# Optimization experiments

Hardware: AMD Instinct MI355X
Metric: run time of the kernel (lower is better)

The kernel has to match this reference:

```python
import jax, jax.numpy as jnp
import numpy as np

N, E, H, ED, GD = 100000, 1600000, 128, 64, 64
LN_EPS = 1e-5


def setup_inputs() -> dict:
    key = jax.random.key(0)
    ks = jax.random.split(key, 16)
    s = lambda d: 1.0 / np.sqrt(d)
    return {
        "node_state": jax.random.normal(ks[0], (N, H), jnp.float32),
        "edge_index": jax.random.randint(ks[1], (2, E), 0, N, jnp.int64),
        "edge_state": jax.random.normal(ks[2], (E, ED), jnp.float32),
        "global_state": jax.random.normal(ks[3], (GD,), jnp.float32),
        "msg_w1": jax.random.normal(ks[4], (H + ED + GD, H), jnp.float32) * s(H + ED + GD),
        "msg_b1": jnp.zeros((H,), jnp.float32),
        "msg_w2": jax.random.normal(ks[5], (H, H), jnp.float32) * s(H),
        "msg_b2": jnp.zeros((H,), jnp.float32),
        "upd_w1": jax.random.normal(ks[6], (2 * H + GD, H), jnp.float32) * s(2 * H + GD),
        "upd_b1": jnp.zeros((H,), jnp.float32),
        "upd_w2": jax.random.normal(ks[7], (H, H), jnp.float32) * s(H),
        "upd_b2": jnp.zeros((H,), jnp.float32),
        "ln_gamma": jnp.ones((H,), jnp.float32),
        "ln_beta": jnp.zeros((H,), jnp.float32),
    }


def _mlp(x, w1, b1, w2, b2):
    return jax.nn.relu(x @ w1 + b1) @ w2 + b2


def reference(node_state, edge_index, edge_state, global_state,
              msg_w1, msg_b1, msg_w2, msg_b2,
              upd_w1, upd_b1, upd_w2, upd_b2,
              ln_gamma, ln_beta):
    src, dst = edge_index[0], edge_index[1]
    num_nodes = node_state.shape[0]
    num_edges = src.shape[0]

    global_edges = jnp.broadcast_to(global_state, (num_edges, global_state.shape[0]))
    message_input = jnp.concatenate([node_state[src], edge_state, global_edges], axis=-1)
    messages = _mlp(message_input, msg_w1, msg_b1, msg_w2, msg_b2)  # [E, H]

    aggregated = jax.ops.segment_sum(messages, dst, num_segments=num_nodes)  # [N, H]
    degree = jax.ops.segment_sum(jnp.ones((num_edges,), node_state.dtype), dst,
                                 num_segments=num_nodes)  # [N]
    aggregated = aggregated / jnp.maximum(degree, 1.0)[:, None]

    global_nodes = jnp.broadcast_to(global_state, (num_nodes, global_state.shape[0]))
    update_input = jnp.concatenate([node_state, aggregated, global_nodes], axis=-1)
    delta = _mlp(update_input, upd_w1, upd_b1, upd_w2, upd_b2)

    x = node_state + delta
    mu = jnp.mean(x, axis=-1, keepdims=True)
    var = jnp.mean(jnp.square(x - mu), axis=-1, keepdims=True)
    return (x - mu) * jax.lax.rsqrt(var + LN_EPS) * ln_gamma + ln_beta
```

## Files before the change

### kernel.cpp

```cpp
#include <hip/hip_runtime.h>
#include <hip/hip_bf16.h>
#include <stdint.h>

#define NN 100000
#define NE 1600000

typedef __attribute__((ext_vector_type(4))) float f32x4;
typedef __attribute__((ext_vector_type(8))) __bf16 bf16x8;
typedef __attribute__((ext_vector_type(8))) short s16x8;
typedef __attribute__((ext_vector_type(4))) unsigned int u32x4;

__device__ __forceinline__ unsigned short f2bf(float f) {
  unsigned int u = __builtin_bit_cast(unsigned int, f);
  u += 0x7fffu + ((u >> 16) & 1u);
  return (unsigned short)(u >> 16);
}

__device__ __forceinline__ f32x4 mfma16(bf16x8 a, bf16x8 b, f32x4 c) {
  return __builtin_amdgcn_mfma_f32_16x16x32_bf16(a, b, c, 0, 0, 0);
}

__global__ void convert_kernel(const float* __restrict__ w1, const float* __restrict__ w2,
                               const float* __restrict__ g,
                               unsigned short* __restrict__ w1b, unsigned short* __restrict__ w2b,
                               unsigned short* __restrict__ gb)
{
  const int tid = blockIdx.x * 256 + threadIdx.x;
  if (tid < 256 * 128) w1b[tid] = f2bf(w1[tid]);
  if (tid < 128 * 128) w2b[tid] = f2bf(w2[tid]);
  if (tid < 64) gb[tid] = f2bf(g[tid]);
}

__global__ __launch_bounds__(256, 2) void edge_kernel(
    const int* __restrict__ ei,
    const float* __restrict__ edge_state,
    const float* __restrict__ node_state,
    const unsigned short* __restrict__ w1b,
    const unsigned short* __restrict__ w2b,
    const float* __restrict__ bias1g,
    const float* __restrict__ bias2g,
    const unsigned short* __restrict__ gb,
    float* __restrict__ agg,
    float* __restrict__ deg)
{
  __shared__ unsigned short sX[64 * 256];
  __shared__ unsigned short sH[64 * 128];
  __shared__ int sDst[64];

  const int t = threadIdx.x;
  const int lane = t & 63;
  const int wv = t >> 6;
  const int l15 = lane & 15;
  const int lq = lane >> 4;

  bf16x8 b1f[8][2], b2f[4][2];
  float bs1[2], bs2[2];
  for (int n = 0; n < 2; ++n) {
    const int col = wv * 32 + n * 16 + l15;
    bs1[n] = bias1g[col];
    bs2[n] = bias2g[col];
    for (int ks = 0; ks < 8; ++ks) {
      const int k0 = ks * 32 + lq * 8;
      s16x8 v;
#pragma unroll
      for (int j = 0; j < 8; ++j) v[j] = (short)w1b[(k0 + j) * 128 + col];
      b1f[ks][n] = __builtin_bit_cast(bf16x8, v);
    }
    for (int ks = 0; ks < 4; ++ks) {
      const int k0 = ks * 32 + lq * 8;
      s16x8 v;
#pragma unroll
      for (int j = 0; j < 8; ++j) v[j] = (short)w2b[(k0 + j) * 128 + col];
      b2f[ks][n] = __builtin_bit_cast(bf16x8, v);
    }
  }

  const int r = t >> 2;
  const int p = t & 3;
  const int rs = r & 7;

  for (int tile = blockIdx.x; tile < NE / 64; tile += gridDim.x) {
    __syncthreads();
    const int e0 = tile * 64;

    const int src = ei[e0 + r];
    if (p == 0) {
      const int d = ei[NE + e0 + r];
      sDst[r] = d;
      atomicAdd(&deg[d], 1.0f);
    }
    {
      const f32x4* nsv = (const f32x4*)(node_state + (size_t)src * 128 + p * 32);
#pragma unroll
      for (int j = 0; j < 4; ++j) {
        f32x4 x0 = nsv[2 * j], x1 = nsv[2 * j + 1];
        unsigned short buf[8];
#pragma unroll
        for (int i = 0; i < 4; ++i) { buf[i] = f2bf(x0[i]); buf[4 + i] = f2bf(x1[i]); }
        const int c = p * 4 + j;
        *(u32x4*)((char*)sX + r * 512 + ((c ^ rs) * 16)) = *(u32x4*)buf;
      }
    }
    {
      const f32x4* es = (const f32x4*)(edge_state + (size_t)e0 * 64 + r * 64 + p * 16);
      f32x4 e0v = es[0], e1v = es[1], e2v = es[2], e3v = es[3];
      unsigned short bufa[8], bufb[8];
#pragma unroll
      for (int i = 0; i < 4; ++i) {
        bufa[i] = f2bf(e0v[i]); bufa[4 + i] = f2bf(e1v[i]);
        bufb[i] = f2bf(e2v[i]); bufb[4 + i] = f2bf(e3v[i]);
      }
      const int c = 16 + 2 * p;
      *(u32x4*)((char*)sX + r * 512 + ((c ^ rs) * 16)) = *(u32x4*)bufa;
      *(u32x4*)((char*)sX + r * 512 + (((c + 1) ^ rs) * 16)) = *(u32x4*)bufb;
    }
    {
      const u32x4* g = (const u32x4*)(gb + p * 16);
      const int c = 24 + 2 * p;
      *(u32x4*)((char*)sX + r * 512 + ((c ^ rs) * 16)) = g[0];
      *(u32x4*)((char*)sX + r * 512 + (((c + 1) ^ rs) * 16)) = g[1];
    }
    __syncthreads();

    f32x4 acc[4][2];
#pragma unroll
    for (int m = 0; m < 4; ++m)
#pragma unroll
      for (int n = 0; n < 2; ++n)
        acc[m][n] = (f32x4){bs1[n], bs1[n], bs1[n], bs1[n]};
#pragma unroll
    for (int ks = 0; ks < 8; ++ks) {
      bf16x8 a[4];
#pragma unroll
      for (int m = 0; m < 4; ++m) {
        const int row = m * 16 + l15;
        a[m] = *(const bf16x8*)((const char*)sX + row * 512 + (((4 * ks + lq) ^ (row & 7)) * 16));
      }
#pragma unroll
      for (int m = 0; m < 4; ++m)
#pragma unroll
        for (int n = 0; n < 2; ++n)
          acc[m][n] = mfma16(a[m], b1f[ks][n], acc[m][n]);
    }
#pragma unroll
    for (int m = 0; m < 4; ++m)
#pragma unroll
      for (int n = 0; n < 2; ++n)
#pragma unroll
        for (int i = 0; i < 4; ++i) {
          const int row = m * 16 + lq * 4 + i;
          const int col = wv * 32 + n * 16 + l15;
          float v = acc[m][n][i];
          v = v > 0.f ? v : 0.f;
          *(unsigned short*)((char*)sH + row * 256 +
                             ((((col >> 3) ^ (row & 7)) * 16) + (col & 7) * 2)) = f2bf(v);
        }
    __syncthreads();

    f32x4 acc2[4][2];
#pragma unroll
    for (int m = 0; m < 4; ++m)
#pragma unroll
      for (int n = 0; n < 2; ++n)
        acc2[m][n] = (f32x4){bs2[n], bs2[n], bs2[n], bs2[n]};
#pragma unroll
    for (int ks = 0; ks < 4; ++ks) {
      bf16x8 a[4];
#pragma unroll
      for (int m = 0; m < 4; ++m) {
        const int row = m * 16 + l15;
        a[m] = *(const bf16x8*)((const char*)sH + row * 256 + (((4 * ks + lq) ^ (row & 7)) * 16));
      }
#pragma unroll
      for (int m = 0; m < 4; ++m)
#pragma unroll
        for (int n = 0; n < 2; ++n)
          acc2[m][n] = mfma16(a[m], b2f[ks][n], acc2[m][n]);
    }
#pragma unroll
    for (int m = 0; m < 4; ++m)
#pragma unroll
      for (int i = 0; i < 4; ++i) {
        const int row = m * 16 + lq * 4 + i;
        const int d = sDst[row];
#pragma unroll
        for (int n = 0; n < 2; ++n) {
          const int col = wv * 32 + n * 16 + l15;
          atomicAdd(&agg[(size_t)d * 128 + col], acc2[m][n][i]);
        }
      }
  }
}

__global__ __launch_bounds__(128, 3) void upd1_kernel(
    const float* __restrict__ node_state,
    const float* __restrict__ agg,
    const float* __restrict__ deg,
    const float* __restrict__ u1,
    const float* __restrict__ b1,
    const float* __restrict__ gs,
    float* __restrict__ h1out)
{
  const int n = blockIdx.x * 128 + threadIdx.x;
  const bool act = n < NN;
  const size_t row = (size_t)(act ? n : 0) * 128;

  f32x4 acc[32];
#pragma unroll
  for (int c = 0; c < 32; ++c) acc[c] = *(const f32x4*)(b1 + 4 * c);

  const float rdeg = act ? (1.0f / fmaxf(deg[n], 1.0f)) : 0.0f;

  for (int k4 = 0; k4 < 32; ++k4) {
    const f32x4 x = *(const f32x4*)(node_state + row + 4 * k4);
#pragma unroll
    for (int kk = 0; kk < 4; ++kk) {
      const float xk = x[kk];
      const float* wr = u1 + (size_t)(4 * k4 + kk) * 128;
#pragma unroll
      for (int c = 0; c < 32; ++c) acc[c] += xk * *(const f32x4*)(wr + 4 * c);
    }
  }
  for (int k4 = 0; k4 < 32; ++k4) {
    const f32x4 x = *(const f32x4*)(agg + row + 4 * k4);
#pragma unroll
    for (int kk = 0; kk < 4; ++kk) {
      const float xk = x[kk] * rdeg;
      const float* wr = u1 + (size_t)(128 + 4 * k4 + kk) * 128;
#pragma unroll
      for (int c = 0; c < 32; ++c) acc[c] += xk * *(const f32x4*)(wr + 4 * c);
    }
  }
  for (int k = 0; k < 64; ++k) {
    const float xk = gs[k];
    const float* wr = u1 + (size_t)(256 + k) * 128;
#pragma unroll
    for (int c = 0; c < 32; ++c) acc[c] += xk * *(const f32x4*)(wr + 4 * c);
  }

  if (act) {
    float* o = h1out + (size_t)n * 128;
#pragma unroll
    for (int c = 0; c < 32; ++c) {
      f32x4 v = acc[c];
#pragma unroll
      for (int i = 0; i < 4; ++i) v[i] = v[i] > 0.f ? v[i] : 0.f;
      *(f32x4*)(o + 4 * c) = v;
    }
  }
}

__global__ __launch_bounds__(128, 3) void upd2_kernel(
    const float* __restrict__ node_state,
    const float* __restrict__ h1,
    const float* __restrict__ u2,
    const float* __restrict__ b2,
    const float* __restrict__ lng,
    const float* __restrict__ lnb,
    float* __restrict__ out)
{
  const int n = blockIdx.x * 128 + threadIdx.x;
  const bool act = n < NN;
  const size_t row = (size_t)(act ? n : 0) * 128;

  f32x4 acc[32];
#pragma unroll
  for (int c = 0; c < 32; ++c) acc[c] = *(const f32x4*)(b2 + 4 * c);

  for (int k4 = 0; k4 < 32; ++k4) {
    const f32x4 h = *(const f32x4*)(h1 + row + 4 * k4);
#pragma unroll
    for (int kk = 0; kk < 4; ++kk) {
      const float hk = h[kk];
      const float* wr = u2 + (size_t)(4 * k4 + kk) * 128;
#pragma unroll
      for (int c = 0; c < 32; ++c) acc[c] += hk * *(const f32x4*)(wr + 4 * c);
    }
  }

  if (act) {
    float s = 0.f, s2 = 0.f;
#pragma unroll
    for (int c = 0; c < 32; ++c) {
      const f32x4 nd = *(const f32x4*)(node_state + row + 4 * c);
      f32x4 x = nd + acc[c];
      acc[c] = x;
#pragma unroll
      for (int i = 0; i < 4; ++i) { s += x[i]; s2 += x[i] * x[i]; }
    }
    const float mu = s * (1.0f / 128.0f);
    float var = s2 * (1.0f / 128.0f) - mu * mu;
    var = var < 0.f ? 0.f : var;
    const float rstd = rsqrtf(var + 1e-5f);
    float* o = out + (size_t)n * 128;
#pragma unroll
    for (int c = 0; c < 32; ++c) {
      const f32x4 g = *(const f32x4*)(lng + 4 * c);
      const f32x4 b = *(const f32x4*)(lnb + 4 * c);
      f32x4 x = acc[c];
#pragma unroll
      for (int i = 0; i < 4; ++i) x[i] = (x[i] - mu) * rstd * g[i] + b[i];
      *(f32x4*)(o + 4 * c) = x;
    }
  }
}

extern "C" void kernel_launch(void* const* d_in, const int* in_sizes, int n_in,
                              void* d_out, int out_size, void* d_ws, size_t ws_size,
                              hipStream_t stream)
{
  const float* node_state = (const float*)d_in[0];
  const int* ei           = (const int*)d_in[1];
  const float* edge_state = (const float*)d_in[2];
  const float* gstate     = (const float*)d_in[3];
  const float* msg_w1     = (const float*)d_in[4];
  const float* msg_b1     = (const float*)d_in[5];
  const float* msg_w2     = (const float*)d_in[6];
  const float* msg_b2     = (const float*)d_in[7];
  const float* upd_w1     = (const float*)d_in[8];
  const float* upd_b1     = (const float*)d_in[9];
  const float* upd_w2     = (const float*)d_in[10];
  const float* upd_b2     = (const float*)d_in[11];
  const float* ln_g       = (const float*)d_in[12];
  const float* ln_b       = (const float*)d_in[13];

  char* ws = (char*)d_ws;
  float* agg              = (float*)(ws + 0);
  float* deg              = (float*)(ws + 51200000);
  float* h1buf            = (float*)(ws + 51600000);
  unsigned short* w1b     = (unsigned short*)(ws + 102800000);
  unsigned short* w2b     = (unsigned short*)(ws + 102865536);
  unsigned short* gb      = (unsigned short*)(ws + 102898304);
  (void)ws_size; (void)in_sizes; (void)n_in; (void)out_size;

  hipMemsetAsync(ws, 0, 51600000, stream);
  hipLaunchKernelGGL(convert_kernel, dim3(128), dim3(256), 0, stream,
                     msg_w1, msg_w2, gstate, w1b, w2b, gb);
  hipLaunchKernelGGL(edge_kernel, dim3(512), dim3(256), 0, stream,
                     ei, edge_state, node_state, w1b, w2b, msg_b1, msg_b2, gb, agg, deg);
  hipLaunchKernelGGL(upd1_kernel, dim3((NN + 127) / 128), dim3(128), 0, stream,
                     node_state, agg, deg, upd_w1, upd_b1, gstate, h1buf);
  hipLaunchKernelGGL(upd2_kernel, dim3((NN + 127) / 128), dim3(128), 0, stream,
                     node_state, h1buf, upd_w2, upd_b2, ln_g, ln_b, (float*)d_out);
}
```

Before: 1.167 ms.

## Sort edges by destination via CSR and pre-reduce messages before atomics

Builds a destination-sorted edge permutation (histogram, single-block scan, atomic scatter) and has the edge kernel process edges in that order. Each tile stages its messages in shared memory and run-length sums them per destination column, so there are far fewer float atomics into the aggregate buffer. Degree now comes from the integer histogram. The cost is three extra kernels, one of them a serial single-block scan, plus gathered rather than streaming edge_state reads. Occupancy is raised to 3 blocks per SM with a larger grid.

```diff
diff --git a/kernel.cpp b/kernel.cpp
--- a/kernel.cpp
+++ b/kernel.cpp
@@ -31,21 +31,74 @@
   if (tid < 64) gb[tid] = f2bf(g[tid]);
 }
 
-__global__ __launch_bounds__(256, 2) void edge_kernel(
+__global__ void hist_kernel(const int* __restrict__ ei, int* __restrict__ cnt)
+{
+  int i = blockIdx.x * 256 + threadIdx.x;
+  const int stride = gridDim.x * 256;
+  for (; i < NE; i += stride) atomicAdd(&cnt[ei[NE + i]], 1);
+}
+
+__global__ __launch_bounds__(1024) void scan_kernel(const int* __restrict__ cnt,
+                                                    int* __restrict__ row_start,
+                                                    int* __restrict__ cursor)
+{
+  __shared__ int part[1024];
+  const int t = threadIdx.x;
+  const int chunk = (NN + 1023) / 1024;
+  const int base = t * chunk;
+  int s = 0;
+  for (int i = 0; i < chunk; ++i) {
+    const int idx = base + i;
+    if (idx < NN) s += cnt[idx];
+  }
+  part[t] = s;
+  __syncthreads();
+  for (int off = 1; off < 1024; off <<= 1) {
+    int v = (t >= off) ? part[t - off] : 0;
+    __syncthreads();
+    part[t] += v;
+    __syncthreads();
+  }
+  int run = (t == 0) ? 0 : part[t - 1];
+  for (int i = 0; i < chunk; ++i) {
+    const int idx = base + i;
+    if (idx < NN) {
+      row_start[idx] = run;
+      cursor[idx] = run;
+      run += cnt[idx];
+    }
+  }
+}
+
+__global__ void scatter_kernel(const int* __restrict__ ei, int* __restrict__ cursor,
+                               int* __restrict__ csr)
+{
+  int i = blockIdx.x * 256 + threadIdx.x;
+  const int stride = gridDim.x * 256;
+  for (; i < NE; i += stride) {
+    const int d = ei[NE + i];
+    const int pos = atomicAdd(&cursor[d], 1);
+    csr[pos] = i;
+  }
+}
+
+__global__ __launch_bounds__(256, 3) void edge_kernel(
     const int* __restrict__ ei,
     const float* __restrict__ edge_state,
     const float* __restrict__ node_state,
+    const int* __restrict__ csr,
     const unsigned short* __restrict__ w1b,
     const unsigned short* __restrict__ w2b,
     const float* __restrict__ bias1g,
     const float* __restrict__ bias2g,
     const unsigned short* __restrict__ gb,
-    float* __restrict__ agg,
-    float* __restrict__ deg)
+    float* __restrict__ agg)
 {
   __shared__ unsigned short sX[64 * 256];
   __shared__ unsigned short sH[64 * 128];
   __shared__ int sDst[64];
+  __shared__ int sEid[64];
+  float* sMsgF = (float*)sX;
 
   const int t = threadIdx.x;
   const int lane = t & 63;
@@ -81,14 +134,12 @@
 
   for (int tile = blockIdx.x; tile < NE / 64; tile += gridDim.x) {
     __syncthreads();
-    const int e0 = tile * 64;
-
-    const int src = ei[e0 + r];
-    if (p == 0) {
-      const int d = ei[NE + e0 + r];
-      sDst[r] = d;
-      atomicAdd(&deg[d], 1.0f);
-    }
+    if (t < 64) sEid[t] = csr[tile * 64 + t];
+    __syncthreads();
+
+    const int e = sEid[r];
+    const int src = ei[e];
+    if (p == 0) sDst[r] = ei[NE + e];
     {
       const f32x4* nsv = (const f32x4*)(node_state + (size_t)src * 128 + p * 32);
 #pragma unroll
@@ -102,7 +153,7 @@
       }
     }
     {
-      const f32x4* es = (const f32x4*)(edge_state + (size_t)e0 * 64 + r * 64 + p * 16);
+      const f32x4* es = (const f32x4*)(edge_state + (size_t)e * 64 + p * 16);
       f32x4 e0v = es[0], e1v = es[1], e2v = es[2], e3v = es[3];
       unsigned short bufa[8], bufb[8];
 #pragma unroll
@@ -180,22 +231,39 @@
 #pragma unroll
     for (int m = 0; m < 4; ++m)
 #pragma unroll
-      for (int i = 0; i < 4; ++i) {
-        const int row = m * 16 + lq * 4 + i;
-        const int d = sDst[row];
-#pragma unroll
-        for (int n = 0; n < 2; ++n) {
+      for (int n = 0; n < 2; ++n)
+#pragma unroll
+        for (int i = 0; i < 4; ++i) {
+          const int row = m * 16 + lq * 4 + i;
           const int col = wv * 32 + n * 16 + l15;
-          atomicAdd(&agg[(size_t)d * 128 + col], acc2[m][n][i]);
+          sMsgF[row * 128 + (col ^ row)] = acc2[m][n][i];
         }
+    __syncthreads();
+
+    {
+      const int col = t & 127;
+      const int base = (t >> 7) * 32;
+      float run = 0.f;
+      int prevd = sDst[base];
+      for (int j = 0; j < 32; ++j) {
+        const int rr = base + j;
+        const int d = sDst[rr];
+        if (d != prevd) {
+          atomicAdd(&agg[(size_t)prevd * 128 + col], run);
+          run = 0.f;
+          prevd = d;
+        }
+        run += sMsgF[rr * 128 + (col ^ rr)];
       }
+      atomicAdd(&agg[(size_t)prevd * 128 + col], run);
+    }
   }
 }
 
 __global__ __launch_bounds__(128, 3) void upd1_kernel(
     const float* __restrict__ node_state,
     const float* __restrict__ agg,
-    const float* __restrict__ deg,
+    const int* __restrict__ cnt,
     const float* __restrict__ u1,
     const float* __restrict__ b1,
     const float* __restrict__ gs,
@@ -209,7 +277,7 @@
 #pragma unroll
   for (int c = 0; c < 32; ++c) acc[c] = *(const f32x4*)(b1 + 4 * c);
 
-  const float rdeg = act ? (1.0f / fmaxf(deg[n], 1.0f)) : 0.0f;
+  const float rdeg = act ? (1.0f / (float)max(cnt[n], 1)) : 0.0f;
 
   for (int k4 = 0; k4 < 32; ++k4) {
     const f32x4 x = *(const f32x4*)(node_state + row + 4 * k4);
@@ -326,8 +394,11 @@
 
   char* ws = (char*)d_ws;
   float* agg              = (float*)(ws + 0);
-  float* deg              = (float*)(ws + 51200000);
+  int* cnt                = (int*)(ws + 51200000);
   float* h1buf            = (float*)(ws + 51600000);
+  int* csr                = (int*)(ws + 51600000);
+  int* row_start          = (int*)(ws + 58000000);
+  int* cursor             = (int*)(ws + 58400000);
   unsigned short* w1b     = (unsigned short*)(ws + 102800000);
   unsigned short* w2b     = (unsigned short*)(ws + 102865536);
   unsigned short* gb      = (unsigned short*)(ws + 102898304);
@@ -336,10 +407,13 @@
   hipMemsetAsync(ws, 0, 51600000, stream);
   hipLaunchKernelGGL(convert_kernel, dim3(128), dim3(256), 0, stream,
                      msg_w1, msg_w2, gstate, w1b, w2b, gb);
-  hipLaunchKernelGGL(edge_kernel, dim3(512), dim3(256), 0, stream,
-                     ei, edge_state, node_state, w1b, w2b, msg_b1, msg_b2, gb, agg, deg);
+  hipLaunchKernelGGL(hist_kernel, dim3(2048), dim3(256), 0, stream, ei, cnt);
+  hipLaunchKernelGGL(scan_kernel, dim3(1), dim3(1024), 0, stream, cnt, row_start, cursor);
+  hipLaunchKernelGGL(scatter_kernel, dim3(2048), dim3(256), 0, stream, ei, cursor, csr);
+  hipLaunchKernelGGL(edge_kernel, dim3(768), dim3(256), 0, stream,
+                     ei, edge_state, node_state, csr, w1b, w2b, msg_b1, msg_b2, gb, agg);
   hipLaunchKernelGGL(upd1_kernel, dim3((NN + 127) / 128), dim3(128), 0, stream,
-                     node_state, agg, deg, upd_w1, upd_b1, gstate, h1buf);
+                     node_state, agg, cnt, upd_w1, upd_b1, gstate, h1buf);
   hipLaunchKernelGGL(upd2_kernel, dim3((NN + 127) / 128), dim3(128), 0, stream,
                      node_state, h1buf, upd_w2, upd_b2, ln_g, ln_b, (float*)d_out);
 }
```

Result: slower. 2.390 ms (+104.7%).

## Replace global atomic scatter with bucketed fp8 message staging and LDS aggregation

Applied to the files above, without the earlier changes.

The edge kernel no longer does float atomicAdds into the global aggregate. It converts each message to fp8, appends it to a per-destination bucket of 64 nodes (capacity 1536 per bucket) and records the low destination bits. A new agg kernel then sums each bucket in shared memory and writes the aggregate and integer degree once per node. Node state is also pre-converted to bf16, and the next tile's gathers are prefetched in registers to overlap loads with MFMA work. The trade-offs are fp8 quantisation error in the messages, edges silently dropped if a bucket overflows its fixed capacity, and a large extra workspace buffer for the staged messages.

```diff
diff --git a/kernel.cpp b/kernel.cpp
--- a/kernel.cpp
+++ b/kernel.cpp
@@ -4,8 +4,11 @@
 
 #define NN 100000
 #define NE 1600000
+#define NBK 1563
+#define BCAP 1536
 
 typedef __attribute__((ext_vector_type(4))) float f32x4;
+typedef __attribute__((ext_vector_type(2))) float f32x2;
 typedef __attribute__((ext_vector_type(8))) __bf16 bf16x8;
 typedef __attribute__((ext_vector_type(8))) short s16x8;
 typedef __attribute__((ext_vector_type(4))) unsigned int u32x4;
@@ -20,28 +23,33 @@
   return __builtin_amdgcn_mfma_f32_16x16x32_bf16(a, b, c, 0, 0, 0);
 }
 
-__global__ void convert_kernel(const float* __restrict__ w1, const float* __restrict__ w2,
+__global__ void convert_kernel(const float* __restrict__ ns,
+                               const float* __restrict__ w1, const float* __restrict__ w2,
                                const float* __restrict__ g,
+                               unsigned short* __restrict__ node_bf,
                                unsigned short* __restrict__ w1b, unsigned short* __restrict__ w2b,
                                unsigned short* __restrict__ gb)
 {
   const int tid = blockIdx.x * 256 + threadIdx.x;
+  const int stride = gridDim.x * 256;
+  for (int i = tid; i < NN * 128; i += stride) node_bf[i] = f2bf(ns[i]);
   if (tid < 256 * 128) w1b[tid] = f2bf(w1[tid]);
   if (tid < 128 * 128) w2b[tid] = f2bf(w2[tid]);
   if (tid < 64) gb[tid] = f2bf(g[tid]);
 }
 
-__global__ __launch_bounds__(256, 2) void edge_kernel(
+__global__ __launch_bounds__(256, 3) void edge_msg_kernel(
     const int* __restrict__ ei,
     const float* __restrict__ edge_state,
-    const float* __restrict__ node_state,
+    const unsigned short* __restrict__ node_bf,
     const unsigned short* __restrict__ w1b,
     const unsigned short* __restrict__ w2b,
     const float* __restrict__ bias1g,
     const float* __restrict__ bias2g,
     const unsigned short* __restrict__ gb,
-    float* __restrict__ agg,
-    float* __restrict__ deg)
+    int* __restrict__ bcur,
+    unsigned int* __restrict__ msgs,
+    unsigned char* __restrict__ dst8)
 {
   __shared__ unsigned short sX[64 * 256];
   __shared__ unsigned short sH[64 * 128];
@@ -79,48 +87,70 @@
   const int p = t & 3;
   const int rs = r & 7;
 
-  for (int tile = blockIdx.x; tile < NE / 64; tile += gridDim.x) {
+  u32x4 gR0, gR1;
+  {
+    const u32x4* g = (const u32x4*)(gb + p * 16);
+    gR0 = g[0]; gR1 = g[1];
+  }
+
+  const int grid = gridDim.x;
+  const int NT = NE / 64;
+
+  u32x4 pfN[4];
+  f32x4 pfE[4];
+  int srcNext, dstNext, dstCur;
+  {
+    const int e0 = blockIdx.x * 64 + r;
+    const int s0 = ei[e0];
+    dstCur = ei[NE + e0];
+    const u32x4* nb = (const u32x4*)(node_bf + (size_t)s0 * 128);
+    const f32x4* es = (const f32x4*)(edge_state + (size_t)e0 * 64);
+#pragma unroll
+    for (int j = 0; j < 4; ++j) { pfN[j] = nb[p * 4 + j]; pfE[j] = es[p * 4 + j]; }
+    const int e1 = min((blockIdx.x + grid) * 64 + r, NE - 1);
+    srcNext = ei[e1];
+    dstNext = ei[NE + e1];
+  }
+
+  for (int tile = blockIdx.x; tile < NT; tile += grid) {
     __syncthreads();
-    const int e0 = tile * 64;
-
-    const int src = ei[e0 + r];
-    if (p == 0) {
-      const int d = ei[NE + e0 + r];
-      sDst[r] = d;
-      atomicAdd(&deg[d], 1.0f);
+
+    if (p == 0) sDst[r] = dstCur;
+#pragma unroll
+    for (int j = 0; j < 4; ++j) {
+      const int c = p * 4 + j;
+      *(u32x4*)((char*)sX + r * 512 + ((c ^ rs) * 16)) = pfN[j];
     }
     {
-      const f32x4* nsv = (const f32x4*)(node_state + (size_t)src * 128 + p * 32);
-#pragma unroll
-      for (int j = 0; j < 4; ++j) {
-        f32x4 x0 = nsv[2 * j], x1 = nsv[2 * j + 1];
-        unsigned short buf[8];
-#pragma unroll
-        for (int i = 0; i < 4; ++i) { buf[i] = f2bf(x0[i]); buf[4 + i] = f2bf(x1[i]); }
-        const int c = p * 4 + j;
-        *(u32x4*)((char*)sX + r * 512 + ((c ^ rs) * 16)) = *(u32x4*)buf;
-      }
-    }
-    {
-      const f32x4* es = (const f32x4*)(edge_state + (size_t)e0 * 64 + r * 64 + p * 16);
-      f32x4 e0v = es[0], e1v = es[1], e2v = es[2], e3v = es[3];
       unsigned short bufa[8], bufb[8];
 #pragma unroll
       for (int i = 0; i < 4; ++i) {
-        bufa[i] = f2bf(e0v[i]); bufa[4 + i] = f2bf(e1v[i]);
-        bufb[i] = f2bf(e2v[i]); bufb[4 + i] = f2bf(e3v[i]);
+        bufa[i] = f2bf(pfE[0][i]); bufa[4 + i] = f2bf(pfE[1][i]);
+        bufb[i] = f2bf(pfE[2][i]); bufb[4 + i] = f2bf(pfE[3][i]);
       }
       const int c = 16 + 2 * p;
       *(u32x4*)((char*)sX + r * 512 + ((c ^ rs) * 16)) = *(u32x4*)bufa;
       *(u32x4*)((char*)sX + r * 512 + (((c + 1) ^ rs) * 16)) = *(u32x4*)bufb;
     }
     {
-      const u32x4* g = (const u32x4*)(gb + p * 16);
       const int c = 24 + 2 * p;
-      *(u32x4*)((char*)sX + r * 512 + ((c ^ rs) * 16)) = g[0];
-      *(u32x4*)((char*)sX + r * 512 + (((c + 1) ^ rs) * 16)) = g[1];
+      *(u32x4*)((char*)sX + r * 512 + ((c ^ rs) * 16)) = gR0;
+      *(u32x4*)((char*)sX + r * 512 + (((c + 1) ^ rs) * 16)) = gR1;
     }
     __syncthreads();
+
+    {
+      const int tn = tile + grid;
+      const int eN = min(tn * 64 + r, NE - 1);
+      const u32x4* nb = (const u32x4*)(node_bf + (size_t)srcNext * 128);
+      const f32x4* es = (const f32x4*)(edge_state + (size_t)eN * 64);
+#pragma unroll
+      for (int j = 0; j < 4; ++j) { pfN[j] = nb[p * 4 + j]; pfE[j] = es[p * 4 + j]; }
+      dstCur = dstNext;
+      const int e2 = min((tn + grid) * 64 + r, NE - 1);
+      srcNext = ei[e2];
+      dstNext = ei[NE + e2];
+    }
 
     f32x4 acc[4][2];
 #pragma unroll
@@ -180,22 +210,108 @@
 #pragma unroll
     for (int m = 0; m < 4; ++m)
 #pragma unroll
-      for (int i = 0; i < 4; ++i) {
-        const int row = m * 16 + lq * 4 + i;
-        const int d = sDst[row];
-#pragma unroll
-        for (int n = 0; n < 2; ++n) {
+      for (int n = 0; n < 2; ++n)
+#pragma unroll
+        for (int i = 0; i < 4; ++i) {
+          const int row = m * 16 + lq * 4 + i;
           const int col = wv * 32 + n * 16 + l15;
-          atomicAdd(&agg[(size_t)d * 128 + col], acc2[m][n][i]);
+          *(unsigned short*)((char*)sX + row * 256 +
+                             ((((col >> 3) ^ (row & 7)) * 16) + (col & 7) * 2)) = f2bf(acc2[m][n][i]);
         }
+    __syncthreads();
+
+    {
+      const int d = sDst[r];
+      int gpos = -1;
+      if (p == 0) {
+        const int b = d >> 6;
+        const int slot = atomicAdd(&bcur[b], 1);
+        gpos = (slot < BCAP) ? b * BCAP + slot : -1;
+        if (gpos >= 0) dst8[gpos] = (unsigned char)(d & 63);
       }
-  }
+      gpos = __shfl(gpos, lane & 60);
+      if (gpos >= 0) {
+        unsigned int ww[8];
+#pragma unroll
+        for (int j = 0; j < 4; ++j) {
+          const int cc = 4 * p + j;
+          const u32x4 ch = *(const u32x4*)((const char*)sX + r * 256 + ((cc ^ rs) * 16));
+          float f[8];
+#pragma unroll
+          for (int q = 0; q < 4; ++q) {
+            f[2 * q]     = __builtin_bit_cast(float, ch[q] << 16);
+            f[2 * q + 1] = __builtin_bit_cast(float, ch[q] & 0xffff0000u);
+          }
+          unsigned int w0 = __builtin_amdgcn_cvt_pk_fp8_f32(f[0], f[1], 0, false);
+          w0 = __builtin_amdgcn_cvt_pk_fp8_f32(f[2], f[3], w0, true);
+          unsigned int w1 = __builtin_amdgcn_cvt_pk_fp8_f32(f[4], f[5], 0, false);
+          w1 = __builtin_amdgcn_cvt_pk_fp8_f32(f[6], f[7], w1, true);
+          ww[2 * j] = w0; ww[2 * j + 1] = w1;
+        }
+        unsigned int* mrow = msgs + (size_t)gpos * 32 + 8 * p;
+        *(u32x4*)(mrow)     = (u32x4){ww[0], ww[1], ww[2], ww[3]};
+        *(u32x4*)(mrow + 4) = (u32x4){ww[4], ww[5], ww[6], ww[7]};
+      }
+    }
+  }
+}
+
+__global__ __launch_bounds__(256) void agg_kernel(
+    const unsigned int* __restrict__ msgs,
+    const unsigned char* __restrict__ dst8,
+    const int* __restrict__ bcur,
+    float* __restrict__ agg,
+    int* __restrict__ deg)
+{
+  __shared__ float sAgg[64 * 128];
+  __shared__ int sDeg[64];
+
+  const int b = blockIdx.x;
+  const int t = threadIdx.x;
+
+#pragma unroll
+  for (int k = 0; k < 8; ++k)
+    *(f32x4*)(sAgg + (k * 256 + t) * 4) = (f32x4){0.f, 0.f, 0.f, 0.f};
+  if (t < 64) sDeg[t] = 0;
+  __syncthreads();
+
+  const int n = min(bcur[b], BCAP);
+  const size_t base = (size_t)b * BCAP;
+
+  for (int i0 = 0; i0 < n; i0 += 8) {
+    const int row = i0 + (t >> 5);
+    const int dw = t & 31;
+    if (row < n) {
+      const unsigned int m = msgs[(base + row) * 32 + dw];
+      const int d = dst8[base + row];
+      const f32x2 lo = __builtin_amdgcn_cvt_pk_f32_fp8((int)m, false);
+      const f32x2 hi = __builtin_amdgcn_cvt_pk_f32_fp8((int)m, true);
+      float* rowp = sAgg + d * 128 + dw * 4;
+      atomicAdd(rowp + 0, lo[0]);
+      atomicAdd(rowp + 1, lo[1]);
+      atomicAdd(rowp + 2, hi[0]);
+      atomicAdd(rowp + 3, hi[1]);
+      if (dw == 0) atomicAdd(&sDeg[d], 1);
+    }
+  }
+  __syncthreads();
+
+  const int r = t >> 2;
+  const int p = t & 3;
+  const int node = b * 64 + r;
+  if (node < NN) {
+#pragma unroll
+    for (int k = 0; k < 8; ++k)
+      *(f32x4*)(agg + (size_t)node * 128 + p * 32 + k * 4) =
+          *(const f32x4*)(sAgg + r * 128 + p * 32 + k * 4);
+  }
+  if (t < 64 && b * 64 + t < NN) deg[b * 64 + t] = sDeg[t];
 }
 
 __global__ __launch_bounds__(128, 3) void upd1_kernel(
     const float* __restrict__ node_state,
     const float* __restrict__ agg,
-    const float* __restrict__ deg,
+    const int* __restrict__ cnt,
     const float* __restrict__ u1,
     const float* __restrict__ b1,
     const float* __restrict__ gs,
@@ -209,7 +325,7 @@
 #pragma unroll
   for (int c = 0; c < 32; ++c) acc[c] = *(const f32x4*)(b1 + 4 * c);
 
-  const float rdeg = act ? (1.0f / fmaxf(deg[n], 1.0f)) : 0.0f;
+  const float rdeg = act ? (1.0f / (float)max(cnt[n], 1)) : 0.0f;
 
   for (int k4 = 0; k4 < 32; ++k4) {
     const f32x4 x = *(const f32x4*)(node_state + row + 4 * k4);
@@ -326,18 +442,25 @@
 
   char* ws = (char*)d_ws;
   float* agg              = (float*)(ws + 0);
-  float* deg              = (float*)(ws + 51200000);
-  float* h1buf            = (float*)(ws + 51600000);
-  unsigned short* w1b     = (unsigned short*)(ws + 102800000);
-  unsigned short* w2b     = (unsigned short*)(ws + 102865536);
-  unsigned short* gb      = (unsigned short*)(ws + 102898304);
+  unsigned short* node_bf = (unsigned short*)(ws + 0);
+  int* deg                = (int*)(ws + 51200000);
+  int* bcur               = (int*)(ws + 51600000);
+  unsigned short* w1b     = (unsigned short*)(ws + 51608192);
+  unsigned short* w2b     = (unsigned short*)(ws + 51673728);
+  unsigned short* gb      = (unsigned short*)(ws + 51706496);
+  unsigned char* dst8     = (unsigned char*)(ws + 51706752);
+  unsigned int* msgs      = (unsigned int*)(ws + 54108160);
+  float* h1buf            = (float*)(ws + 54108160);
   (void)ws_size; (void)in_sizes; (void)n_in; (void)out_size;
 
-  hipMemsetAsync(ws, 0, 51600000, stream);
-  hipLaunchKernelGGL(convert_kernel, dim3(128), dim3(256), 0, stream,
-                     msg_w1, msg_w2, gstate, w1b, w2b, gb);
-  hipLaunchKernelGGL(edge_kernel, dim3(512), dim3(256), 0, stream,
-                     ei, edge_state, node_state, w1b, w2b, msg_b1, msg_b2, gb, agg, deg);
+  hipMemsetAsync(bcur, 0, 8192, stream);
+  hipLaunchKernelGGL(convert_kernel, dim3(2048), dim3(256), 0, stream,
+                     node_state, msg_w1, msg_w2, gstate, node_bf, w1b, w2b, gb);
+  hipLaunchKernelGGL(edge_msg_kernel, dim3(768), dim3(256), 0, stream,
+                     ei, edge_state, node_bf, w1b, w2b, msg_b1, msg_b2, gb,
+                     bcur, msgs, dst8);
+  hipLaunchKernelGGL(agg_kernel, dim3(NBK), dim3(256), 0, stream,
+                     msgs, dst8, bcur, agg, deg);
   hipLaunchKernelGGL(upd1_kernel, dim3((NN + 127) / 128), dim3(128), 0, stream,
                      node_state, agg, deg, upd_w1, upd_b1, gstate, h1buf);
   hipLaunchKernelGGL(upd2_kernel, dim3((NN + 127) / 128), dim3(128), 0, stream,
```

Result: slower. 2.485 ms (+112.8%).

## Pre-convert node states to bf16 and software-prefetch next edge tile

Applied to the files above, without the earlier changes.

Node states are converted to bf16 once in the convert kernel, which halves the gathered bytes per edge and removes the per-edge conversion. The edge kernel now prefetches the next tile's indices, node rows and edge features into registers while the current tile's MFMAs run. The sH buffer now aliases sX, with an extra barrier, so LDS use drops and occupancy can rise (launch bounds 4, grid 1024). This adds register pressure and one more sync per tile, plus an extra pass over node_state.

```diff
diff --git a/kernel.cpp b/kernel.cpp
--- a/kernel.cpp
+++ b/kernel.cpp
@@ -20,21 +20,25 @@
   return __builtin_amdgcn_mfma_f32_16x16x32_bf16(a, b, c, 0, 0, 0);
 }
 
-__global__ void convert_kernel(const float* __restrict__ w1, const float* __restrict__ w2,
+__global__ void convert_kernel(const float* __restrict__ ns,
+                               const float* __restrict__ w1, const float* __restrict__ w2,
                                const float* __restrict__ g,
+                               unsigned short* __restrict__ node_bf,
                                unsigned short* __restrict__ w1b, unsigned short* __restrict__ w2b,
                                unsigned short* __restrict__ gb)
 {
   const int tid = blockIdx.x * 256 + threadIdx.x;
+  const int stride = gridDim.x * 256;
+  for (int i = tid; i < NN * 128; i += stride) node_bf[i] = f2bf(ns[i]);
   if (tid < 256 * 128) w1b[tid] = f2bf(w1[tid]);
   if (tid < 128 * 128) w2b[tid] = f2bf(w2[tid]);
   if (tid < 64) gb[tid] = f2bf(g[tid]);
 }
 
-__global__ __launch_bounds__(256, 2) void edge_kernel(
+__global__ __launch_bounds__(256, 4) void edge_kernel(
     const int* __restrict__ ei,
     const float* __restrict__ edge_state,
-    const float* __restrict__ node_state,
+    const unsigned short* __restrict__ node_bf,
     const unsigned short* __restrict__ w1b,
     const unsigned short* __restrict__ w2b,
     const float* __restrict__ bias1g,
@@ -44,8 +48,8 @@
     float* __restrict__ deg)
 {
   __shared__ unsigned short sX[64 * 256];
-  __shared__ unsigned short sH[64 * 128];
   __shared__ int sDst[64];
+  unsigned short* sH = sX;
 
   const int t = threadIdx.x;
   const int lane = t & 63;
@@ -79,48 +83,73 @@
   const int p = t & 3;
   const int rs = r & 7;
 
-  for (int tile = blockIdx.x; tile < NE / 64; tile += gridDim.x) {
+  u32x4 gR0, gR1;
+  {
+    const u32x4* g = (const u32x4*)(gb + p * 16);
+    gR0 = g[0]; gR1 = g[1];
+  }
+
+  const int grid = gridDim.x;
+  const int NT = NE / 64;
+
+  u32x4 pfN[4];
+  f32x4 pfE[4];
+  int srcNext, dstNext, dstCur;
+  {
+    const int e0 = blockIdx.x * 64 + r;
+    const int s0 = ei[e0];
+    dstCur = ei[NE + e0];
+    const u32x4* nb = (const u32x4*)(node_bf + (size_t)s0 * 128);
+    const f32x4* es = (const f32x4*)(edge_state + (size_t)e0 * 64);
+#pragma unroll
+    for (int j = 0; j < 4; ++j) { pfN[j] = nb[p * 4 + j]; pfE[j] = es[p * 4 + j]; }
+    const int e1 = min((blockIdx.x + grid) * 64 + r, NE - 1);
+    srcNext = ei[e1];
+    dstNext = ei[NE + e1];
+  }
+
+  for (int tile = blockIdx.x; tile < NT; tile += grid) {
     __syncthreads();
-    const int e0 = tile * 64;
-
-    const int src = ei[e0 + r];
+
     if (p == 0) {
-      const int d = ei[NE + e0 + r];
-      sDst[r] = d;
-      atomicAdd(&deg[d], 1.0f);
+      sDst[r] = dstCur;
+      atomicAdd(&deg[dstCur], 1.0f);
+    }
+#pragma unroll
+    for (int j = 0; j < 4; ++j) {
+      const int c = p * 4 + j;
+      *(u32x4*)((char*)sX + r * 512 + ((c ^ rs) * 16)) = pfN[j];
     }
     {
-      const f32x4* nsv = (const f32x4*)(node_state + (size_t)src * 128 + p * 32);
-#pragma unroll
-      for (int j = 0; j < 4; ++j) {
-        f32x4 x0 = nsv[2 * j], x1 = nsv[2 * j + 1];
-        unsigned short buf[8];
-#pragma unroll
-        for (int i = 0; i < 4; ++i) { buf[i] = f2bf(x0[i]); buf[4 + i] = f2bf(x1[i]); }
-        const int c = p * 4 + j;
-        *(u32x4*)((char*)sX + r * 512 + ((c ^ rs) * 16)) = *(u32x4*)buf;
-      }
-    }
-    {
-      const f32x4* es = (const f32x4*)(edge_state + (size_t)e0 * 64 + r * 64 + p * 16);
-      f32x4 e0v = es[0], e1v = es[1], e2v = es[2], e3v = es[3];
       unsigned short bufa[8], bufb[8];
 #pragma unroll
       for (int i = 0; i < 4; ++i) {
-        bufa[i] = f2bf(e0v[i]); bufa[4 + i] = f2bf(e1v[i]);
-        bufb[i] = f2bf(e2v[i]); bufb[4 + i] = f2bf(e3v[i]);
+        bufa[i] = f2bf(pfE[0][i]); bufa[4 + i] = f2bf(pfE[1][i]);
+        bufb[i] = f2bf(pfE[2][i]); bufb[4 + i] = f2bf(pfE[3][i]);
       }
       const int c = 16 + 2 * p;
       *(u32x4*)((char*)sX + r * 512 + ((c ^ rs) * 16)) = *(u32x4*)bufa;
       *(u32x4*)((char*)sX + r * 512 + (((c + 1) ^ rs) * 16)) = *(u32x4*)bufb;
     }
     {
-      const u32x4* g = (const u32x4*)(gb + p * 16);
       const int c = 24 + 2 * p;
-      *(u32x4*)((char*)sX + r * 512 + ((c ^ rs) * 16)) = g[0];
-      *(u32x4*)((char*)sX + r * 512 + (((c + 1) ^ rs) * 16)) = g[1];
+      *(u32x4*)((char*)sX + r * 512 + ((c ^ rs) * 16)) = gR0;
+      *(u32x4*)((char*)sX + r * 512 + (((c + 1) ^ rs) * 16)) = gR1;
     }
     __syncthreads();
+
+    {
+      const int tn = tile + grid;
+      const int eN = min(tn * 64 + r, NE - 1);
+      const u32x4* nb = (const u32x4*)(node_bf + (size_t)srcNext * 128);
+      const f32x4* es = (const f32x4*)(edge_state + (size_t)eN * 64);
+#pragma unroll
+      for (int j = 0; j < 4; ++j) { pfN[j] = nb[p * 4 + j]; pfE[j] = es[p * 4 + j]; }
+      dstCur = dstNext;
+      const int e2 = min((tn + grid) * 64 + r, NE - 1);
+      srcNext = ei[e2];
+      dstNext = ei[NE + e2];
+    }
 
     f32x4 acc[4][2];
 #pragma unroll
@@ -142,6 +171,8 @@
         for (int n = 0; n < 2; ++n)
           acc[m][n] = mfma16(a[m], b1f[ks][n], acc[m][n]);
     }
+    __syncthreads();
+
 #pragma unroll
     for (int m = 0; m < 4; ++m)
 #pragma unroll
@@ -327,17 +358,18 @@
   char* ws = (char*)d_ws;
   float* agg              = (float*)(ws + 0);
   float* deg              = (float*)(ws + 51200000);
-  float* h1buf            = (float*)(ws + 51600000);
-  unsigned short* w1b     = (unsigned short*)(ws + 102800000);
-  unsigned short* w2b     = (unsigned short*)(ws + 102865536);
-  unsigned short* gb      = (unsigned short*)(ws + 102898304);
+  unsigned short* node_bf = (unsigned short*)(ws + 51600000);
+  unsigned short* w1b     = (unsigned short*)(ws + 77200000);
+  unsigned short* w2b     = (unsigned short*)(ws + 77265536);
+  unsigned short* gb      = (unsigned short*)(ws + 77298304);
+  float* h1buf            = (float*)(ws + 77300000);
   (void)ws_size; (void)in_sizes; (void)n_in; (void)out_size;
 
   hipMemsetAsync(ws, 0, 51600000, stream);
-  hipLaunchKernelGGL(convert_kernel, dim3(128), dim3(256), 0, stream,
-                     msg_w1, msg_w2, gstate, w1b, w2b, gb);
-  hipLaunchKernelGGL(edge_kernel, dim3(512), dim3(256), 0, stream,
-                     ei, edge_state, node_state, w1b, w2b, msg_b1, msg_b2, gb, agg, deg);
+  hipLaunchKernelGGL(convert_kernel, dim3(2048), dim3(256), 0, stream,
+                     node_state, msg_w1, msg_w2, gstate, node_bf, w1b, w2b, gb);
+  hipLaunchKernelGGL(edge_kernel, dim3(1024), dim3(256), 0, stream,
+                     ei, edge_state, node_bf, w1b, w2b, msg_b1, msg_b2, gb, agg, deg);
   hipLaunchKernelGGL(upd1_kernel, dim3((NN + 127) / 128), dim3(128), 0, stream,
                      node_state, agg, deg, upd_w1, upd_b1, gstate, h1buf);
   hipLaunchKernelGGL(upd2_kernel, dim3((NN + 127) / 128), dim3(128), 0, stream,
```

Measured after the change: 1.369 ms. 17.3% more time.
